# Optimization experiments

Measured on AMD Instinct MI355X. Metric: run time of the kernel, lower is better.

The kernel has to match this reference:

```python
import jax, jax.numpy as jnp
import numpy as np

N, E, H, D, FE = 50000, 400000, 4, 64, 64  # nodes, edges, heads, per-head dim, edge feat dim
NEG_SLOPE = 0.2


def setup_inputs() -> dict:
    key = jax.random.key(0)
    ks = jax.random.split(key, 18)
    def p(k, shape, s=0.1):
        return jax.random.normal(k, shape, dtype=jnp.float32) * s
    return dict(
        features=p(ks[0], (N, D), 1.0),
        edge_feat=p(ks[1], (E, FE), 1.0),
        src=jax.random.randint(ks[2], (E,), 0, N),
        dst=jax.random.randint(ks[3], (E,), 0, N),
        # layer 0: in=64 -> H*D=256, residual Linear since 64 != 256
        W0=p(ks[4], (D, H * D)), We0=p(ks[5], (FE, H * D)),
        al0=p(ks[6], (H, D)), ar0=p(ks[7], (H, D)), ae0=p(ks[8], (H, D)),
        b0=p(ks[9], (H * D,)), Wres0=p(ks[10], (D, H * D)),
        # layer 1 (last): in=256 -> H*D=256, residual = identity view
        W1=p(ks[11], (H * D, H * D)), We1=p(ks[12], (FE, H * D)),
        al1=p(ks[13], (H, D)), ar1=p(ks[14], (H, D)), ae1=p(ks[15], (H, D)),
        b1=p(ks[16], (H * D,)),
    )


def _edge_gat_layer(h, ef, src, dst, W, We, al, ar, ae, b, Wres=None):
    n = h.shape[0]
    ft = (h @ W).reshape(n, H, D)          # (N,H,D) projected node feats
    fe = (ef @ We).reshape(-1, H, D)       # (E,H,D) projected edge feats
    el = jnp.sum(ft * al, axis=-1)         # (N,H)
    er = jnp.sum(ft * ar, axis=-1)         # (N,H)
    ee = jnp.sum(fe * ae, axis=-1)         # (E,H)
    e = el[src] + er[dst] + ee             # (E,H)
    e = jnp.where(e > 0, e, NEG_SLOPE * e)  # leaky_relu(0.2)
    # segment softmax over incoming edges of each dst node
    m = jax.ops.segment_max(jax.lax.stop_gradient(e), dst, num_segments=n)
    ex = jnp.exp(e - m[dst])
    den = jax.ops.segment_sum(ex, dst, num_segments=n)
    a = ex / den[dst]                      # (E,H) attention
    out = jax.ops.segment_sum(ft[src] * a[:, :, None], dst, num_segments=n)  # (N,H,D)
    res = (h @ Wres).reshape(n, H, D) if Wres is not None else h.reshape(n, H, D)
    return out + res + b.reshape(1, H, D)


def reference(features, edge_feat, src, dst,
              W0, We0, al0, ar0, ae0, b0, Wres0,
              W1, We1, al1, ar1, ae1, b1):
    h = _edge_gat_layer(features, edge_feat, src, dst, W0, We0, al0, ar0, ae0, b0, Wres0)
    h = jax.nn.elu(h.reshape(N, H * D))    # flatten heads + ELU between layers
    h = _edge_gat_layer(h, edge_feat, src, dst, W1, We1, al1, ar1, ae1, b1)
    return h.mean(axis=1)                  # (N, D) mean over heads on last layer
```

## Files before the change

kernel.cpp:

```cpp
#include <hip/hip_runtime.h>
#include <hip/hip_bf16.h>

#define NN 50000
#define EE 400000
#define NB 196

typedef __bf16 bf16_8 __attribute__((ext_vector_type(8)));
typedef __bf16 bf16_2 __attribute__((ext_vector_type(2)));
typedef float f32x4 __attribute__((ext_vector_type(4)));
typedef float f32x2 __attribute__((ext_vector_type(2)));

__device__ inline f32x2 bf2(unsigned u) {
  f32x2 r;
  r.x = __uint_as_float(u << 16);
  r.y = __uint_as_float(u & 0xffff0000u);
  return r;
}

__global__ __launch_bounds__(256) void prep_kernel(
    const float* __restrict__ features, __bf16* __restrict__ fbf,
    const float* __restrict__ W0, const float* __restrict__ Wres0, __bf16* __restrict__ Bt0,
    const float* __restrict__ W1, __bf16* __restrict__ Bt1,
    const float* __restrict__ We0, const float* __restrict__ ae0, float* __restrict__ Ve0,
    const float* __restrict__ We1, const float* __restrict__ ae1, float* __restrict__ Ve1,
    const int* __restrict__ dst, int* __restrict__ cnt) {
  int b = blockIdx.x;
  int t = threadIdx.x;
  if (b < 1563) {
    int i = b * 256 + t;
    if (i < NN * 64 / 8) {
      const float4* p = (const float4*)features + (size_t)i * 2;
      float4 a = p[0], c = p[1];
      bf16_8 v = {(__bf16)a.x, (__bf16)a.y, (__bf16)a.z, (__bf16)a.w,
                  (__bf16)c.x, (__bf16)c.y, (__bf16)c.z, (__bf16)c.w};
      *(bf16_8*)(fbf + (size_t)i * 8) = v;
    }
  } else if (b < 1563 + 128) {
    int idx = (b - 1563) * 256 + t;
    int j = idx >> 6, k = idx & 63;
    float v = (j < 256) ? W0[k * 256 + j] : Wres0[k * 256 + (j - 256)];
    Bt0[idx] = (__bf16)v;
  } else if (b < 1563 + 128 + 256) {
    int idx = (b - 1563 - 128) * 256 + t;
    int j = idx >> 8, k = idx & 255;
    Bt1[idx] = (__bf16)W1[k * 256 + j];
  } else if (b == 1947) {
    int f = t >> 2, h = t & 3;
    float s = 0.f;
    for (int d = 0; d < 64; ++d) s += We0[f * 256 + h * 64 + d] * ae0[h * 64 + d];
    Ve0[f * 4 + h] = s;
  } else if (b == 1948) {
    int f = t >> 2, h = t & 3;
    float s = 0.f;
    for (int d = 0; d < 64; ++d) s += We1[f * 256 + h * 64 + d] * ae1[h * 64 + d];
    Ve1[f * 4 + h] = s;
  } else {
    int e = (b - 1949) * 256 + t;
    if (e < EE) atomicAdd(&cnt[dst[e]], 1);
  }
}

__global__ __launch_bounds__(256) void scan1_kernel(const int* __restrict__ cnt,
                                                    int* __restrict__ scanbuf,
                                                    int* __restrict__ blocksum) {
  __shared__ int s[256];
  int t = threadIdx.x;
  int idx = blockIdx.x * 256 + t;
  int c = (idx < NN) ? cnt[idx] : 0;
  s[t] = c;
  __syncthreads();
  for (int d = 1; d < 256; d <<= 1) {
    int v = (t >= d) ? s[t - d] : 0;
    __syncthreads();
    s[t] += v;
    __syncthreads();
  }
  if (idx < NN) scanbuf[idx] = s[t];
  if (t == 255) blocksum[blockIdx.x] = s[255];
}

__global__ __launch_bounds__(256) void scan2_kernel(const int* __restrict__ blocksum,
                                                    int* __restrict__ blockoff, int nb) {
  __shared__ int s[256];
  int t = threadIdx.x;
  int c = (t < nb) ? blocksum[t] : 0;
  s[t] = c;
  __syncthreads();
  for (int d = 1; d < 256; d <<= 1) {
    int v = (t >= d) ? s[t - d] : 0;
    __syncthreads();
    s[t] += v;
    __syncthreads();
  }
  if (t < nb) blockoff[t] = s[t] - c;
}

__global__ __launch_bounds__(256) void scan3_kernel(const int* __restrict__ scanbuf,
                                                    const int* __restrict__ cnt,
                                                    const int* __restrict__ blockoff,
                                                    int* __restrict__ off,
                                                    int* __restrict__ cur) {
  int idx = blockIdx.x * 256 + threadIdx.x;
  if (idx < NN) {
    int o = blockoff[blockIdx.x] + scanbuf[idx] - cnt[idx];
    off[idx] = o;
    cur[idx] = o;
  }
  if (idx == 0) off[NN] = EE;
}

__global__ __launch_bounds__(256) void fill_kernel(const int* __restrict__ src,
                                                   const int* __restrict__ dst,
                                                   int* __restrict__ cur,
                                                   int* __restrict__ srcc,
                                                   int* __restrict__ pose) {
  int e = blockIdx.x * 256 + threadIdx.x;
  if (e < EE) {
    int p = atomicAdd(&cur[dst[e]], 1);
    srcc[p] = src[e];
    pose[e] = p;
  }
}

__global__ __launch_bounds__(256) void eek_kernel(const float* __restrict__ ef,
                                                  const float* __restrict__ Ve0,
                                                  const float* __restrict__ Ve1,
                                                  float* __restrict__ eeo0,
                                                  float* __restrict__ eeo1) {
  __shared__ float V0[256], V1[256];
  V0[threadIdx.x] = Ve0[threadIdx.x];
  V1[threadIdx.x] = Ve1[threadIdx.x];
  __syncthreads();
  int r = threadIdx.x >> 2, sub = threadIdx.x & 3;
  int e = blockIdx.x * 64 + r;
  if (e >= EE) return;
  float a0 = 0, a1 = 0, a2 = 0, a3 = 0;
  float c0 = 0, c1 = 0, c2 = 0, c3 = 0;
  const float* row = ef + (size_t)e * 64 + sub * 16;
#pragma unroll
  for (int i = 0; i < 16; i += 4) {
    float4 v = *(const float4*)(row + i);
    float xs[4] = {v.x, v.y, v.z, v.w};
#pragma unroll
    for (int j = 0; j < 4; ++j) {
      float x = xs[j];
      int idx = (sub * 16 + i + j) * 4;
      a0 += x * V0[idx + 0]; a1 += x * V0[idx + 1];
      a2 += x * V0[idx + 2]; a3 += x * V0[idx + 3];
      c0 += x * V1[idx + 0]; c1 += x * V1[idx + 1];
      c2 += x * V1[idx + 2]; c3 += x * V1[idx + 3];
    }
  }
#pragma unroll
  for (int o = 1; o < 4; o <<= 1) {
    a0 += __shfl_xor(a0, o); a1 += __shfl_xor(a1, o);
    a2 += __shfl_xor(a2, o); a3 += __shfl_xor(a3, o);
    c0 += __shfl_xor(c0, o); c1 += __shfl_xor(c1, o);
    c2 += __shfl_xor(c2, o); c3 += __shfl_xor(c3, o);
  }
  if (sub == 0) {
    float4 u; u.x = a0; u.y = a1; u.z = a2; u.w = a3;
    float4 w; w.x = c0; w.y = c1; w.z = c2; w.w = c3;
    *(float4*)(eeo0 + (size_t)e * 4) = u;
    *(float4*)(eeo1 + (size_t)e * 4) = w;
  }
}

#define LDK 40
__global__ __launch_bounds__(256) void gemm_kernel(const __bf16* __restrict__ A,
                                                   const __bf16* __restrict__ Bt,
                                                   __bf16* __restrict__ ft,
                                                   __bf16* __restrict__ base,
                                                   const float* __restrict__ bias,
                                                   const float* __restrict__ al,
                                                   const float* __restrict__ ar,
                                                   float* __restrict__ el,
                                                   float* __restrict__ er,
                                                   int M, int K) {
  __shared__ __align__(16) __bf16 Al[64 * LDK];
  __shared__ __align__(16) __bf16 Bl[64 * LDK];
  int tid = threadIdx.x;
  int wav = tid >> 6, lane = tid & 63;
  int quad = lane >> 4, l16 = lane & 15;
  int bm = blockIdx.x * 64;
  int bn = blockIdx.y * 64;
  int sr = tid >> 2;
  int sk = (tid & 3) << 3;

  f32x4 acc[4] = {{0, 0, 0, 0}, {0, 0, 0, 0}, {0, 0, 0, 0}, {0, 0, 0, 0}};

  for (int k0 = 0; k0 < K; k0 += 32) {
    uint4 av = {0, 0, 0, 0};
    int arow = bm + sr;
    if (arow < M) av = *(const uint4*)(A + (size_t)arow * K + k0 + sk);
    uint4 bv = *(const uint4*)(Bt + (size_t)(bn + sr) * K + k0 + sk);
    __syncthreads();
    *(uint4*)&Al[sr * LDK + sk] = av;
    *(uint4*)&Bl[sr * LDK + sk] = bv;
    __syncthreads();
    bf16_8 af = *(const bf16_8*)&Al[(wav * 16 + l16) * LDK + quad * 8];
#pragma unroll
    for (int nt = 0; nt < 4; ++nt) {
      bf16_8 bf = *(const bf16_8*)&Bl[(nt * 16 + l16) * LDK + quad * 8];
      acc[nt] = __builtin_amdgcn_mfma_f32_16x16x32_bf16(af, bf, acc[nt], 0, 0, 0);
    }
  }

  int row0 = bm + wav * 16 + quad * 4;

  if (bn < 256) {
    int hb = bn >> 6;
#pragma unroll
    for (int r = 0; r < 4; ++r) {
      float pl = 0.f, pr = 0.f;
#pragma unroll
      for (int nt = 0; nt < 4; ++nt) {
        float v = acc[nt][r];
        int d = nt * 16 + l16;
        pl += v * al[hb * 64 + d];
        pr += v * ar[hb * 64 + d];
      }
#pragma unroll
      for (int o2 = 8; o2 > 0; o2 >>= 1) {
        pl += __shfl_xor(pl, o2);
        pr += __shfl_xor(pr, o2);
      }
      int row = row0 + r;
      if (l16 == 0 && row < M) {
        el[row * 4 + hb] = pl;
        er[row * 4 + hb] = pr;
      }
    }
  }

#pragma unroll
  for (int nt = 0; nt < 4; ++nt) {
    int col = bn + nt * 16 + l16;
#pragma unroll
    for (int r = 0; r < 4; ++r) {
      int row = row0 + r;
      if (row < M) {
        float v = acc[nt][r];
        if (col < 256)
          ft[(size_t)row * 256 + col] = (__bf16)v;
        else
          base[(size_t)row * 256 + (col - 256)] = (__bf16)(v + bias[col - 256]);
      }
    }
  }
}

__global__ __launch_bounds__(256) void wk_kernel(const int* __restrict__ src,
                                                 const int* __restrict__ dst,
                                                 const int* __restrict__ pose,
                                                 const float* __restrict__ ee,
                                                 const float* __restrict__ el,
                                                 const float* __restrict__ er,
                                                 float* __restrict__ wcsr) {
  int e = blockIdx.x * 256 + threadIdx.x;
  if (e >= EE) return;
  int s = src[e], d = dst[e], p = pose[e];
  float4 z4 = *(const float4*)(ee + (size_t)e * 4);
  float4 e_l = *(const float4*)(el + (size_t)s * 4);
  float4 e_r = *(const float4*)(er + (size_t)d * 4);
  float4 w;
  float z;
  z = e_l.x + e_r.x + z4.x; w.x = __expf(z > 0.f ? z : 0.2f * z);
  z = e_l.y + e_r.y + z4.y; w.y = __expf(z > 0.f ? z : 0.2f * z);
  z = e_l.z + e_r.z + z4.z; w.z = __expf(z > 0.f ? z : 0.2f * z);
  z = e_l.w + e_r.w + z4.w; w.w = __expf(z > 0.f ? z : 0.2f * z);
  *(float4*)(wcsr + (size_t)p * 4) = w;
}

template <int LAYER>
__global__ __launch_bounds__(256) void agg_kernel(const int* __restrict__ off,
                                                  const int* __restrict__ srcc,
                                                  const float* __restrict__ wcsr,
                                                  const __bf16* __restrict__ ft,
                                                  const __bf16* prev,
                                                  const float* __restrict__ bias,
                                                  __bf16* outb,
                                                  float* __restrict__ outf) {
  __shared__ f32x2 wl2[2][4][32];
  __shared__ f32x2 red2[2][4][32];
  int t = threadIdx.x;
  int wav = t >> 6, lane = t & 63;
  int nh = wav >> 1;
  int hf = lane >> 5;
  int head = ((wav & 1) << 1) + hf;
  int k32 = lane & 31;
  int n = blockIdx.x * 2 + nh;
  int beg = off[n], end = off[n + 1];
  int offb = head * 128 + k32 * 4;

  const char* ftb = (const char*)ft;
  f32x2 acc0 = {0.f, 0.f}, acc1 = {0.f, 0.f};
  float denp = 0.f;

  for (int c = beg; c < end; c += 32) {
    int rem = end - c;
    if (rem > 32) rem = 32;
    int sv = 0;
    float wv = 0.f;
    if (k32 < rem) {
      sv = srcc[c + k32];
      wv = wcsr[(size_t)(c + k32) * 4 + head];
    }
    denp += wv;
    f32x2 wd = {wv, wv};
    wl2[nh][head][k32] = wd;
    int kk = 0;
    for (; kk + 4 <= rem; kk += 4) {
      int s0 = __builtin_amdgcn_readlane(sv, kk);
      int s1 = __builtin_amdgcn_readlane(sv, kk + 1);
      int s2 = __builtin_amdgcn_readlane(sv, kk + 2);
      int s3 = __builtin_amdgcn_readlane(sv, kk + 3);
      unsigned u0 = *(const unsigned*)(ftb + (size_t)s0 * 512 + offb);
      unsigned u1 = *(const unsigned*)(ftb + (size_t)s1 * 512 + offb);
      unsigned u2 = *(const unsigned*)(ftb + (size_t)s2 * 512 + offb);
      unsigned u3 = *(const unsigned*)(ftb + (size_t)s3 * 512 + offb);
      f32x2 w0 = wl2[nh][head][kk];
      f32x2 w1 = wl2[nh][head][kk + 1];
      f32x2 w2 = wl2[nh][head][kk + 2];
      f32x2 w3 = wl2[nh][head][kk + 3];
      acc0 = __builtin_elementwise_fma(bf2(u0), w0, acc0);
      acc1 = __builtin_elementwise_fma(bf2(u1), w1, acc1);
      acc0 = __builtin_elementwise_fma(bf2(u2), w2, acc0);
      acc1 = __builtin_elementwise_fma(bf2(u3), w3, acc1);
    }
    for (; kk < rem; ++kk) {
      int s0 = __builtin_amdgcn_readlane(sv, kk);
      unsigned u0 = *(const unsigned*)(ftb + (size_t)s0 * 512 + offb);
      f32x2 w0 = wl2[nh][head][kk];
      acc0 = __builtin_elementwise_fma(bf2(u0), w0, acc0);
    }
  }
#pragma unroll
  for (int m = 16; m; m >>= 1) denp += __shfl_xor(denp, m);

  f32x2 res = {0.f, 0.f};
  if (end > beg) {
    float rd = 1.f / denp;
    res.x = (acc0.x + acc1.x) * rd;
    res.y = (acc0.y + acc1.y) * rd;
  }

  unsigned pu = *(const unsigned*)((const char*)prev + (size_t)n * 512 + offb);
  f32x2 pv = bf2(pu);

  if (LAYER == 0) {
    float vx = res.x + pv.x;
    float vy = res.y + pv.y;
    vx = vx > 0.f ? vx : (__expf(vx) - 1.0f);
    vy = vy > 0.f ? vy : (__expf(vy) - 1.0f);
    bf16_2 o = {(__bf16)vx, (__bf16)vy};
    *(bf16_2*)((char*)outb + (size_t)n * 512 + offb) = o;
  } else {
    f32x2 bv = *(const f32x2*)(bias + head * 64 + 2 * k32);
    f32x2 rv = {res.x + pv.x + bv.x, res.y + pv.y + bv.y};
    red2[nh][head][k32] = rv;
    __syncthreads();
    if ((wav & 1) == 0 && hf == 0) {
      f32x2 a = red2[nh][0][k32];
      f32x2 b = red2[nh][1][k32];
      f32x2 c = red2[nh][2][k32];
      f32x2 d = red2[nh][3][k32];
      f32x2 s = {0.25f * (a.x + b.x + c.x + d.x), 0.25f * (a.y + b.y + c.y + d.y)};
      *(f32x2*)(outf + (size_t)n * 64 + 2 * k32) = s;
    }
  }
}

extern "C" void kernel_launch(void* const* d_in, const int* in_sizes, int n_in,
                              void* d_out, int out_size, void* d_ws, size_t ws_size,
                              hipStream_t stream) {
  const float* features  = (const float*)d_in[0];
  const float* edge_feat = (const float*)d_in[1];
  const int*   src       = (const int*)d_in[2];
  const int*   dst       = (const int*)d_in[3];
  const float* W0    = (const float*)d_in[4];
  const float* We0   = (const float*)d_in[5];
  const float* al0   = (const float*)d_in[6];
  const float* ar0   = (const float*)d_in[7];
  const float* ae0   = (const float*)d_in[8];
  const float* b0    = (const float*)d_in[9];
  const float* Wres0 = (const float*)d_in[10];
  const float* W1    = (const float*)d_in[11];
  const float* We1   = (const float*)d_in[12];
  const float* al1   = (const float*)d_in[13];
  const float* ar1   = (const float*)d_in[14];
  const float* ae1   = (const float*)d_in[15];
  const float* b1    = (const float*)d_in[16];
  float* out = (float*)d_out;

  char* ws = (char*)d_ws;
  size_t o = 0;
  auto alloc = [&](size_t bytes) {
    void* p = ws + o;
    o = (o + bytes + 255) & ~(size_t)255;
    return p;
  };
  int*    cnt      = (int*)alloc((size_t)NN * 4);
  int*    scanbuf  = (int*)alloc((size_t)NN * 4);
  int*    blocksum = (int*)alloc(256 * 4);
  int*    blockoff = (int*)alloc(256 * 4);
  int*    off      = (int*)alloc((size_t)(NN + 1) * 4);
  int*    cur      = (int*)alloc((size_t)NN * 4);
  int*    srcc     = (int*)alloc((size_t)EE * 4);
  int*    pose     = (int*)alloc((size_t)EE * 4);
  float*  eeo0     = (float*)alloc((size_t)EE * 4 * 4);
  float*  eeo1     = (float*)alloc((size_t)EE * 4 * 4);
  float*  wcsr     = (float*)alloc((size_t)EE * 4 * 4);
  float*  el       = (float*)alloc((size_t)NN * 4 * 4);
  float*  er       = (float*)alloc((size_t)NN * 4 * 4);
  float*  Ve0      = (float*)alloc(256 * 4);
  float*  Ve1      = (float*)alloc(256 * 4);
  __bf16* Bt0      = (__bf16*)alloc((size_t)512 * 64 * 2);
  __bf16* Bt1      = (__bf16*)alloc((size_t)256 * 256 * 2);
  __bf16* fbf      = (__bf16*)alloc((size_t)NN * 64 * 2);
  __bf16* ft       = (__bf16*)alloc((size_t)NN * 256 * 2);
  __bf16* base     = (__bf16*)alloc((size_t)NN * 256 * 2);
  __bf16* h1       = base;

  const int EB = (EE + 255) / 256;
  const int MG = (NN + 63) / 64;

  hipMemsetAsync(cnt, 0, (size_t)NN * 4, stream);
  prep_kernel<<<1949 + EB, 256, 0, stream>>>(features, fbf, W0, Wres0, Bt0, W1, Bt1,
                                             We0, ae0, Ve0, We1, ae1, Ve1, dst, cnt);
  scan1_kernel<<<NB, 256, 0, stream>>>(cnt, scanbuf, blocksum);
  scan2_kernel<<<1, 256, 0, stream>>>(blocksum, blockoff, NB);
  scan3_kernel<<<NB, 256, 0, stream>>>(scanbuf, cnt, blockoff, off, cur);
  fill_kernel<<<EB, 256, 0, stream>>>(src, dst, cur, srcc, pose);
  eek_kernel<<<(EE + 63) / 64, 256, 0, stream>>>(edge_feat, Ve0, Ve1, eeo0, eeo1);

  gemm_kernel<<<dim3(MG, 8), 256, 0, stream>>>(fbf, Bt0, ft, base, b0, al0, ar0, el, er, NN, 64);
  wk_kernel<<<EB, 256, 0, stream>>>(src, dst, pose, eeo0, el, er, wcsr);
  agg_kernel<0><<<NN / 2, 256, 0, stream>>>(off, srcc, wcsr, ft, base, nullptr, h1, nullptr);

  gemm_kernel<<<dim3(MG, 4), 256, 0, stream>>>(h1, Bt1, ft, nullptr, nullptr, al1, ar1, el, er, NN, 256);
  wk_kernel<<<EB, 256, 0, stream>>>(src, dst, pose, eeo1, el, er, wcsr);
  agg_kernel<1><<<NN / 2, 256, 0, stream>>>(off, srcc, wcsr, ft, h1, b1, nullptr, out);
}
```

Before: 410.2 us.

## Merge CSR scan, fill and edge-score kernels into one cooperative launch

Replaces the three scan kernels, the CSR fill kernel and the edge-attention projection kernel with a single cooperative-groups kernel that uses grid.sync between the scan phases and grid-strided loops for the fill and edge work. This removes four kernel launches and their gaps from the preprocessing chain. Separately, the aggregation inner loop gains an 8-way unrolled gather stage ahead of the 4-way one, to put more independent loads in flight. The cooperative launch needs all 1024 blocks resident at once, and the grid barriers add their own sync cost.

```diff
diff --git a/kernel.cpp b/kernel.cpp
--- a/kernel.cpp
+++ b/kernel.cpp
@@ -1,9 +1,13 @@
 #include <hip/hip_runtime.h>
 #include <hip/hip_bf16.h>
+#include <hip/hip_cooperative_groups.h>
+
+namespace cg = cooperative_groups;
 
 #define NN 50000
 #define EE 400000
 #define NB 196
+#define COOPB 1024
 
 typedef __bf16 bf16_8 __attribute__((ext_vector_type(8)));
 typedef __bf16 bf16_2 __attribute__((ext_vector_type(2)));
@@ -60,109 +64,105 @@
   }
 }
 
-__global__ __launch_bounds__(256) void scan1_kernel(const int* __restrict__ cnt,
-                                                    int* __restrict__ scanbuf,
-                                                    int* __restrict__ blocksum) {
+__global__ __launch_bounds__(256) void csr_eek_kernel(
+    const int* __restrict__ cnt, int* __restrict__ scanbuf,
+    int* __restrict__ blocksum, int* __restrict__ blockoff,
+    int* __restrict__ off, int* __restrict__ cur,
+    const int* __restrict__ src, const int* __restrict__ dst,
+    int* __restrict__ srcc, int* __restrict__ pose,
+    const float* __restrict__ ef, const float* __restrict__ Ve0,
+    const float* __restrict__ Ve1, float* __restrict__ eeo0,
+    float* __restrict__ eeo1) {
+  cg::grid_group grid = cg::this_grid();
   __shared__ int s[256];
+  __shared__ float V0[256], V1[256];
   int t = threadIdx.x;
-  int idx = blockIdx.x * 256 + t;
-  int c = (idx < NN) ? cnt[idx] : 0;
-  s[t] = c;
-  __syncthreads();
-  for (int d = 1; d < 256; d <<= 1) {
-    int v = (t >= d) ? s[t - d] : 0;
+  int bid = blockIdx.x;
+
+  if (bid < NB) {
+    int idx = bid * 256 + t;
+    int c = (idx < NN) ? cnt[idx] : 0;
+    s[t] = c;
     __syncthreads();
-    s[t] += v;
+    for (int d = 1; d < 256; d <<= 1) {
+      int v = (t >= d) ? s[t - d] : 0;
+      __syncthreads();
+      s[t] += v;
+      __syncthreads();
+    }
+    if (idx < NN) scanbuf[idx] = s[t];
+    if (t == 255) blocksum[bid] = s[255];
+  }
+  grid.sync();
+
+  if (bid == 0) {
+    int c = (t < NB) ? blocksum[t] : 0;
+    s[t] = c;
     __syncthreads();
-  }
-  if (idx < NN) scanbuf[idx] = s[t];
-  if (t == 255) blocksum[blockIdx.x] = s[255];
-}
-
-__global__ __launch_bounds__(256) void scan2_kernel(const int* __restrict__ blocksum,
-                                                    int* __restrict__ blockoff, int nb) {
-  __shared__ int s[256];
-  int t = threadIdx.x;
-  int c = (t < nb) ? blocksum[t] : 0;
-  s[t] = c;
-  __syncthreads();
-  for (int d = 1; d < 256; d <<= 1) {
-    int v = (t >= d) ? s[t - d] : 0;
-    __syncthreads();
-    s[t] += v;
-    __syncthreads();
-  }
-  if (t < nb) blockoff[t] = s[t] - c;
-}
-
-__global__ __launch_bounds__(256) void scan3_kernel(const int* __restrict__ scanbuf,
-                                                    const int* __restrict__ cnt,
-                                                    const int* __restrict__ blockoff,
-                                                    int* __restrict__ off,
-                                                    int* __restrict__ cur) {
-  int idx = blockIdx.x * 256 + threadIdx.x;
-  if (idx < NN) {
-    int o = blockoff[blockIdx.x] + scanbuf[idx] - cnt[idx];
-    off[idx] = o;
-    cur[idx] = o;
-  }
-  if (idx == 0) off[NN] = EE;
-}
-
-__global__ __launch_bounds__(256) void fill_kernel(const int* __restrict__ src,
-                                                   const int* __restrict__ dst,
-                                                   int* __restrict__ cur,
-                                                   int* __restrict__ srcc,
-                                                   int* __restrict__ pose) {
-  int e = blockIdx.x * 256 + threadIdx.x;
-  if (e < EE) {
+    for (int d = 1; d < 256; d <<= 1) {
+      int v = (t >= d) ? s[t - d] : 0;
+      __syncthreads();
+      s[t] += v;
+      __syncthreads();
+    }
+    if (t < NB) blockoff[t] = s[t] - c;
+  }
+  grid.sync();
+
+  if (bid < NB) {
+    int idx = bid * 256 + t;
+    if (idx < NN) {
+      int o = blockoff[bid] + scanbuf[idx] - cnt[idx];
+      off[idx] = o;
+      cur[idx] = o;
+    }
+    if (idx == 0) off[NN] = EE;
+  }
+  grid.sync();
+
+  for (int e = bid * 256 + t; e < EE; e += COOPB * 256) {
     int p = atomicAdd(&cur[dst[e]], 1);
     srcc[p] = src[e];
     pose[e] = p;
   }
-}
-
-__global__ __launch_bounds__(256) void eek_kernel(const float* __restrict__ ef,
-                                                  const float* __restrict__ Ve0,
-                                                  const float* __restrict__ Ve1,
-                                                  float* __restrict__ eeo0,
-                                                  float* __restrict__ eeo1) {
-  __shared__ float V0[256], V1[256];
-  V0[threadIdx.x] = Ve0[threadIdx.x];
-  V1[threadIdx.x] = Ve1[threadIdx.x];
+
+  V0[t] = Ve0[t];
+  V1[t] = Ve1[t];
   __syncthreads();
-  int r = threadIdx.x >> 2, sub = threadIdx.x & 3;
-  int e = blockIdx.x * 64 + r;
-  if (e >= EE) return;
-  float a0 = 0, a1 = 0, a2 = 0, a3 = 0;
-  float c0 = 0, c1 = 0, c2 = 0, c3 = 0;
-  const float* row = ef + (size_t)e * 64 + sub * 16;
-#pragma unroll
-  for (int i = 0; i < 16; i += 4) {
-    float4 v = *(const float4*)(row + i);
-    float xs[4] = {v.x, v.y, v.z, v.w};
-#pragma unroll
-    for (int j = 0; j < 4; ++j) {
-      float x = xs[j];
-      int idx = (sub * 16 + i + j) * 4;
-      a0 += x * V0[idx + 0]; a1 += x * V0[idx + 1];
-      a2 += x * V0[idx + 2]; a3 += x * V0[idx + 3];
-      c0 += x * V1[idx + 0]; c1 += x * V1[idx + 1];
-      c2 += x * V1[idx + 2]; c3 += x * V1[idx + 3];
-    }
-  }
-#pragma unroll
-  for (int o = 1; o < 4; o <<= 1) {
-    a0 += __shfl_xor(a0, o); a1 += __shfl_xor(a1, o);
-    a2 += __shfl_xor(a2, o); a3 += __shfl_xor(a3, o);
-    c0 += __shfl_xor(c0, o); c1 += __shfl_xor(c1, o);
-    c2 += __shfl_xor(c2, o); c3 += __shfl_xor(c3, o);
-  }
-  if (sub == 0) {
-    float4 u; u.x = a0; u.y = a1; u.z = a2; u.w = a3;
-    float4 w; w.x = c0; w.y = c1; w.z = c2; w.w = c3;
-    *(float4*)(eeo0 + (size_t)e * 4) = u;
-    *(float4*)(eeo1 + (size_t)e * 4) = w;
+  int r = t >> 2, sub = t & 3;
+  for (int eb = bid; eb < (EE + 63) / 64; eb += COOPB) {
+    int e = eb * 64 + r;
+    if (e >= EE) continue;
+    float a0 = 0, a1 = 0, a2 = 0, a3 = 0;
+    float c0 = 0, c1 = 0, c2 = 0, c3 = 0;
+    const float* row = ef + (size_t)e * 64 + sub * 16;
+#pragma unroll
+    for (int i = 0; i < 16; i += 4) {
+      float4 v = *(const float4*)(row + i);
+      float xs[4] = {v.x, v.y, v.z, v.w};
+#pragma unroll
+      for (int j = 0; j < 4; ++j) {
+        float x = xs[j];
+        int idx = (sub * 16 + i + j) * 4;
+        a0 += x * V0[idx + 0]; a1 += x * V0[idx + 1];
+        a2 += x * V0[idx + 2]; a3 += x * V0[idx + 3];
+        c0 += x * V1[idx + 0]; c1 += x * V1[idx + 1];
+        c2 += x * V1[idx + 2]; c3 += x * V1[idx + 3];
+      }
+    }
+#pragma unroll
+    for (int o = 1; o < 4; o <<= 1) {
+      a0 += __shfl_xor(a0, o); a1 += __shfl_xor(a1, o);
+      a2 += __shfl_xor(a2, o); a3 += __shfl_xor(a3, o);
+      c0 += __shfl_xor(c0, o); c1 += __shfl_xor(c1, o);
+      c2 += __shfl_xor(c2, o); c3 += __shfl_xor(c3, o);
+    }
+    if (sub == 0) {
+      float4 u; u.x = a0; u.y = a1; u.z = a2; u.w = a3;
+      float4 w; w.x = c0; w.y = c1; w.z = c2; w.w = c3;
+      *(float4*)(eeo0 + (size_t)e * 4) = u;
+      *(float4*)(eeo1 + (size_t)e * 4) = w;
+    }
   }
 }
 
@@ -310,6 +310,40 @@
     f32x2 wd = {wv, wv};
     wl2[nh][head][k32] = wd;
     int kk = 0;
+    for (; kk + 8 <= rem; kk += 8) {
+      int s0 = __builtin_amdgcn_readlane(sv, kk);
+      int s1 = __builtin_amdgcn_readlane(sv, kk + 1);
+      int s2 = __builtin_amdgcn_readlane(sv, kk + 2);
+      int s3 = __builtin_amdgcn_readlane(sv, kk + 3);
+      int s4 = __builtin_amdgcn_readlane(sv, kk + 4);
+      int s5 = __builtin_amdgcn_readlane(sv, kk + 5);
+      int s6 = __builtin_amdgcn_readlane(sv, kk + 6);
+      int s7 = __builtin_amdgcn_readlane(sv, kk + 7);
+      unsigned u0 = *(const unsigned*)(ftb + (size_t)s0 * 512 + offb);
+      unsigned u1 = *(const unsigned*)(ftb + (size_t)s1 * 512 + offb);
+      unsigned u2 = *(const unsigned*)(ftb + (size_t)s2 * 512 + offb);
+      unsigned u3 = *(const unsigned*)(ftb + (size_t)s3 * 512 + offb);
+      unsigned u4 = *(const unsigned*)(ftb + (size_t)s4 * 512 + offb);
+      unsigned u5 = *(const unsigned*)(ftb + (size_t)s5 * 512 + offb);
+      unsigned u6 = *(const unsigned*)(ftb + (size_t)s6 * 512 + offb);
+      unsigned u7 = *(const unsigned*)(ftb + (size_t)s7 * 512 + offb);
+      f32x2 w0 = wl2[nh][head][kk];
+      f32x2 w1 = wl2[nh][head][kk + 1];
+      f32x2 w2 = wl2[nh][head][kk + 2];
+      f32x2 w3 = wl2[nh][head][kk + 3];
+      f32x2 w4 = wl2[nh][head][kk + 4];
+      f32x2 w5 = wl2[nh][head][kk + 5];
+      f32x2 w6 = wl2[nh][head][kk + 6];
+      f32x2 w7 = wl2[nh][head][kk + 7];
+      acc0 = __builtin_elementwise_fma(bf2(u0), w0, acc0);
+      acc1 = __builtin_elementwise_fma(bf2(u1), w1, acc1);
+      acc0 = __builtin_elementwise_fma(bf2(u2), w2, acc0);
+      acc1 = __builtin_elementwise_fma(bf2(u3), w3, acc1);
+      acc0 = __builtin_elementwise_fma(bf2(u4), w4, acc0);
+      acc1 = __builtin_elementwise_fma(bf2(u5), w5, acc1);
+      acc0 = __builtin_elementwise_fma(bf2(u6), w6, acc0);
+      acc1 = __builtin_elementwise_fma(bf2(u7), w7, acc1);
+    }
     for (; kk + 4 <= rem; kk += 4) {
       int s0 = __builtin_amdgcn_readlane(sv, kk);
       int s1 = __builtin_amdgcn_readlane(sv, kk + 1);
@@ -428,11 +462,15 @@
   hipMemsetAsync(cnt, 0, (size_t)NN * 4, stream);
   prep_kernel<<<1949 + EB, 256, 0, stream>>>(features, fbf, W0, Wres0, Bt0, W1, Bt1,
                                              We0, ae0, Ve0, We1, ae1, Ve1, dst, cnt);
-  scan1_kernel<<<NB, 256, 0, stream>>>(cnt, scanbuf, blocksum);
-  scan2_kernel<<<1, 256, 0, stream>>>(blocksum, blockoff, NB);
-  scan3_kernel<<<NB, 256, 0, stream>>>(scanbuf, cnt, blockoff, off, cur);
-  fill_kernel<<<EB, 256, 0, stream>>>(src, dst, cur, srcc, pose);
-  eek_kernel<<<(EE + 63) / 64, 256, 0, stream>>>(edge_feat, Ve0, Ve1, eeo0, eeo1);
+
+  {
+    void* args[] = {(void*)&cnt, (void*)&scanbuf, (void*)&blocksum, (void*)&blockoff,
+                    (void*)&off, (void*)&cur, (void*)&src, (void*)&dst,
+                    (void*)&srcc, (void*)&pose, (void*)&edge_feat, (void*)&Ve0,
+                    (void*)&Ve1, (void*)&eeo0, (void*)&eeo1};
+    hipLaunchCooperativeKernel((const void*)csr_eek_kernel, dim3(COOPB), dim3(256),
+                               args, 0, stream);
+  }
 
   gemm_kernel<<<dim3(MG, 8), 256, 0, stream>>>(fbf, Bt0, ft, base, b0, al0, ar0, el, er, NN, 64);
   wk_kernel<<<EB, 256, 0, stream>>>(src, dst, pose, eeo0, el, er, wcsr);
```

New measurement: 743.8 us. 81.3% more time.
